# Optimization experiments

Measured on AMD Instinct MI355X. Metric: run time of the kernel, lower is better.

The kernel has to match this reference:

```python
import jax, jax.numpy as jnp
import numpy as np

B, N, C = 4, 2048, 1024
H = 16
D = C // H  # head dim = 64

def setup_inputs() -> dict:
    key = jax.random.key(0)
    k1, k2, k3 = jax.random.split(key, 3)
    x = jax.random.normal(k1, (B, N, C), dtype=jnp.float32)
    w_attn = jax.random.normal(k2, (C, 3 * C), dtype=jnp.float32) * (C ** -0.5)
    w_proj = jax.random.normal(k3, (C, C), dtype=jnp.float32) * (C ** -0.5)
    return {"x": x, "w_attn": w_attn, "w_proj": w_proj}

def reference(x, w_attn, w_proj):
    # fused QKV projection (bias=False)
    qkv = jnp.einsum('bnc,cf->bnf', x, w_attn)            # [B,N,3C]
    q, k, v = jnp.split(qkv, 3, axis=-1)                  # each [B,N,C]
    # [B,H,N,D]
    q = q.reshape(B, N, H, D).transpose(0, 2, 1, 3)
    k = k.reshape(B, N, H, D).transpose(0, 2, 1, 3)
    v = v.reshape(B, N, H, D).transpose(0, 2, 1, 3)
    # scaled dot-product attention, non-causal, no mask, dropout_p=0
    scale = 1.0 / jnp.sqrt(jnp.asarray(D, dtype=q.dtype))
    scores = jnp.einsum('bhqd,bhkd->bhqk', q, k) * scale  # [B,H,N,N]
    attn = jax.nn.softmax(scores, axis=-1)
    y = jnp.einsum('bhqk,bhkd->bhqd', attn, v)            # [B,H,N,D]
    y = y.transpose(0, 2, 1, 3).reshape(B, N, C)
    # output projection (bias=False); resid dropout is identity at p=0
    return jnp.einsum('bnc,co->bno', y, w_proj)
```

## Files before the change

### kernel.cpp

```cpp
#include <hip/hip_runtime.h>
#include <hip/hip_bf16.h>

typedef __hip_bfloat16 bf16;
typedef short short8 __attribute__((ext_vector_type(8)));
typedef float f32x4 __attribute__((ext_vector_type(4)));
typedef float f32x16 __attribute__((ext_vector_type(16)));

#define GLOBAL_AS __attribute__((address_space(1)))
#define LDS_AS __attribute__((address_space(3)))

__device__ inline unsigned short f2bf(float x) {
    union { float f; unsigned u; } v; v.f = x;
    unsigned r = v.u + 0x7fffu + ((v.u >> 16) & 1u);
    return (unsigned short)(r >> 16);
}

__device__ inline unsigned pkbf(float a, float b) {
    float2 f; f.x = a; f.y = b;
    union { __hip_bfloat162 h; unsigned u; } c;
    c.h = __float22bfloat162_rn(f);
    return c.u;
}

__device__ inline float fast_exp2(float x) {
#if __has_builtin(__builtin_amdgcn_exp2f)
    return __builtin_amdgcn_exp2f(x);
#else
    return exp2f(x);
#endif
}

__device__ inline void async16(const void* g, void* l) {
    __builtin_amdgcn_global_load_lds((const GLOBAL_AS void*)g, (LDS_AS void*)l, 16, 0, 0);
}


__global__ __launch_bounds__(256) void cvt_f32_bf16(const float* __restrict__ in,
                                                    unsigned short* __restrict__ out, int n4) {
    int i = blockIdx.x * 256 + threadIdx.x;
    if (i < n4) {
        float4 v = ((const float4*)in)[i];
        ushort4 o;
        o.x = f2bf(v.x); o.y = f2bf(v.y); o.z = f2bf(v.z); o.w = f2bf(v.w);
        ((ushort4*)out)[i] = o;
    }
}

__global__ __launch_bounds__(256) void transpose_bf16(const float* __restrict__ in,
                                                      unsigned short* __restrict__ out,
                                                      int R, int Cc) {
    __shared__ float s[32][33];
    int tx = threadIdx.x & 31, ty = threadIdx.x >> 5;
    int c0 = blockIdx.x * 32, r0 = blockIdx.y * 32;
#pragma unroll
    for (int i = 0; i < 4; i++)
        s[ty + i * 8][tx] = in[(size_t)(r0 + ty + i * 8) * Cc + c0 + tx];
    __syncthreads();
#pragma unroll
    for (int i = 0; i < 4; i++)
        out[(size_t)(c0 + ty + i * 8) * R + r0 + tx] = f2bf(s[tx][ty + i * 8]);
}


template <int MODE>
__global__ __launch_bounds__(256) void gemm_bf16(const bf16* __restrict__ A,
                                                 const bf16* __restrict__ Bt,
                                                 unsigned short* __restrict__ outQ,
                                                 unsigned short* __restrict__ outK,
                                                 unsigned short* __restrict__ outV,
                                                 float* __restrict__ outF, float qscale) {
    const int KD = 1024;
    __shared__ __align__(16) char smem[34816];
    bf16* sA = (bf16*)smem;
    bf16* sB = (bf16*)(smem + 16384);
    const int t = threadIdx.x;
    const int w = t >> 6, lane = t & 63, l15 = lane & 15, qd = lane >> 4;
    const int bn = blockIdx.x, bm = blockIdx.y;
    const int wm = (w >> 1) * 64, wn = (w & 1) * 64;
    const int sw = l15 & 7;

    f32x4 acc[4][4];
#pragma unroll
    for (int i = 0; i < 4; i++)
#pragma unroll
        for (int j = 0; j < 4; j++) acc[i][j] = (f32x4){0.f, 0.f, 0.f, 0.f};

    const int rsub = lane >> 3;
    const int csrc = ((lane & 7) ^ rsub) << 3;
    const bf16* Ab = A + (size_t)(bm * 128 + w * 32 + rsub) * KD + csrc;
    const bf16* Bb = Bt + (size_t)(bn * 128 + w * 32 + rsub) * KD + csrc;
    bf16* sAw = sA + (w * 32) * 64;
    bf16* sBw = sB + (w * 32) * 64;

    for (int kt = 0; kt < 16; ++kt) {
#pragma unroll
        for (int j = 0; j < 4; ++j) {
            async16(Ab + (size_t)(j * 8) * KD + kt * 64, sAw + j * 512);
            async16(Bb + (size_t)(j * 8) * KD + kt * 64, sBw + j * 512);
        }
        __syncthreads();
#pragma unroll
        for (int ks = 0; ks < 2; ++ks) {
            const int cphys = (((ks * 4 + qd) ^ sw) << 3);
            short8 af[4], bfv[4];
#pragma unroll
            for (int mi = 0; mi < 4; mi++)
                af[mi] = *(const short8*)&sA[(wm + mi * 16 + l15) * 64 + cphys];
#pragma unroll
            for (int ni = 0; ni < 4; ni++)
                bfv[ni] = *(const short8*)&sB[(wn + ni * 16 + l15) * 64 + cphys];
#pragma unroll
            for (int mi = 0; mi < 4; mi++)
#pragma unroll
                for (int ni = 0; ni < 4; ni++)
                    acc[mi][ni] = __builtin_amdgcn_mfma_f32_16x16x32_bf16(af[mi], bfv[ni],
                                                                          acc[mi][ni], 0, 0, 0);
        }
        __syncthreads();
    }

    if (MODE == 0) {
        unsigned short* sC = (unsigned short*)smem;
        const int part = bn >> 3;
        const int hb = (bn & 7) * 2;
        if (part < 2) {
            const float sc = (part == 0) ? qscale : 1.0f;
            unsigned short* dst = (part == 0) ? outQ : outK;
#pragma unroll
            for (int mi = 0; mi < 4; mi++)
#pragma unroll
                for (int ni = 0; ni < 4; ni++)
#pragma unroll
                    for (int r = 0; r < 4; r++)
                        sC[(wm + mi * 16 + qd * 4 + r) * 136 + wn + ni * 16 + l15] =
                            f2bf(acc[mi][ni][r] * sc);
            __syncthreads();
#pragma unroll
            for (int i = 0; i < 8; i++) {
                const int j = t + i * 256;
                const int row = j >> 4, c16 = j & 15;
                uint4 v = *(const uint4*)&sC[row * 136 + c16 * 8];
                const int m = bm * 128 + row;
                const int b = m >> 11, ns = m & 2047;
                const int h = hb + (c16 >> 3);
                const int dd = (c16 & 7) * 8;
                *(uint4*)&dst[((size_t)(b * 16 + h) * 2048 + ns) * 64 + dd] = v;
            }
        } else {
#pragma unroll
            for (int ni = 0; ni < 4; ni++)
#pragma unroll
                for (int mi = 0; mi < 4; mi++) {
                    uint2 pk;
                    pk.x = (unsigned)f2bf(acc[mi][ni][0]) | ((unsigned)f2bf(acc[mi][ni][1]) << 16);
                    pk.y = (unsigned)f2bf(acc[mi][ni][2]) | ((unsigned)f2bf(acc[mi][ni][3]) << 16);
                    *(uint2*)&sC[(wn + ni * 16 + l15) * 136 + wm + mi * 16 + qd * 4] = pk;
                }
            __syncthreads();
            const int m0b = bm * 128;
            const int b = m0b >> 11, ns0 = m0b & 2047;
#pragma unroll
            for (int i = 0; i < 8; i++) {
                const int j = t + i * 256;
                const int f = j >> 4, tc = j & 15;
                uint4 v = *(const uint4*)&sC[f * 136 + tc * 8];
                const int h = hb + (f >> 6), dd = f & 63;
                *(uint4*)&outV[((size_t)(b * 16 + h) * 64 + dd) * 2048 + ns0 + tc * 8] = v;
            }
        }
    } else {
        float* sF = (float*)smem;
#pragma unroll
        for (int pass = 0; pass < 2; ++pass) {
            if (pass) __syncthreads();
            if ((wm >> 6) == pass) {
#pragma unroll
                for (int mi = 0; mi < 4; mi++)
#pragma unroll
                    for (int ni = 0; ni < 4; ni++)
#pragma unroll
                        for (int r = 0; r < 4; r++)
                            sF[(mi * 16 + qd * 4 + r) * 132 + wn + ni * 16 + l15] =
                                acc[mi][ni][r];
            }
            __syncthreads();
#pragma unroll
            for (int i = 0; i < 8; i++) {
                const int j = t + i * 256;
                const int row = j >> 5, c4 = j & 31;
                float4 v = *(const float4*)&sF[row * 132 + c4 * 4];
                *(float4*)&outF[(size_t)(bm * 128 + pass * 64 + row) * 1024 + bn * 128 +
                                c4 * 4] = v;
            }
        }
    }
}


__global__ __launch_bounds__(256) void attn_kernel(const bf16* __restrict__ Q,
                                                   const bf16* __restrict__ K,
                                                   const bf16* __restrict__ Vt,
                                                   bf16* __restrict__ Y) {
    const int blk = blockIdx.x;
    const int bh = (blk & 7) * 8 + (blk >> 6);
    const int qt = (blk >> 3) & 7;
    const int b = bh >> 4, h16 = bh & 15;
    const int t = threadIdx.x, w = t >> 6, lane = t & 63;
    const int c = lane & 31, hl = lane >> 5;
    const int sw = c & 7;

    __shared__ __align__(16) char smem[36864];
    bf16* sK0 = (bf16*)smem;
    bf16* sK1 = (bf16*)(smem + 8192);
    bf16* sV0 = (bf16*)(smem + 16384);
    bf16* sV1 = (bf16*)(smem + 24576);
    bf16* sO = (bf16*)smem;

    const size_t bhbase = (size_t)bh * 2048 * 64;

    short8 qfA[4], qfB[4];
#pragma unroll
    for (int kc = 0; kc < 4; kc++) {
        qfA[kc] = *(const short8*)(Q + bhbase + (size_t)(qt * 256 + w * 64 + c) * 64 +
                                   kc * 16 + hl * 8);
        qfB[kc] = *(const short8*)(Q + bhbase + (size_t)(qt * 256 + w * 64 + 32 + c) * 64 +
                                   kc * 16 + hl * 8);
    }

    f32x16 z16;
#pragma unroll
    for (int i = 0; i < 16; i++) z16[i] = 0.f;
    f32x16 ot[4];
#pragma unroll
    for (int j = 0; j < 4; j++)
#pragma unroll
        for (int i = 0; i < 16; i++) ot[j][i] = 0.f;
    float lA = 0.f, lB = 0.f;

    const int rsub = lane >> 3;
    const int cg = ((lane & 7) ^ rsub) << 3;
    const bf16* Kb = K + bhbase + (size_t)(w * 16 + rsub) * 64 + cg;
    const bf16* Vb = Vt + bhbase + (size_t)(w * 16 + rsub) * 2048 + cg;
    const int ldsoff = (w * 16) * 64;

#define STAGE(ktile, sKb, sVb)                                                      \
    {                                                                               \
        _Pragma("unroll") for (int j = 0; j < 2; j++) {                             \
            async16(Kb + (size_t)(ktile) * 4096 + j * 512, (sKb) + ldsoff + j * 512); \
            async16(Vb + (size_t)(ktile) * 64 + (size_t)j * 16384,                  \
                    (sVb) + ldsoff + j * 512);                                      \
        }                                                                           \
    }

    auto compute = [&](const bf16* __restrict__ sKb, const bf16* __restrict__ sVb) {
#pragma unroll
        for (int kt2 = 0; kt2 < 2; ++kt2) {
            short8 kf[4];
#pragma unroll
            for (int kc = 0; kc < 4; kc++)
                kf[kc] =
                    *(const short8*)&sKb[(kt2 * 32 + c) * 64 + (((kc * 2 + hl) ^ sw) << 3)];
            __builtin_amdgcn_s_setprio(1);
            f32x16 accA = __builtin_amdgcn_mfma_f32_32x32x16_bf16(kf[0], qfA[0], z16, 0, 0, 0);
            f32x16 accB = __builtin_amdgcn_mfma_f32_32x32x16_bf16(kf[0], qfB[0], z16, 0, 0, 0);
#pragma unroll
            for (int kc = 1; kc < 4; kc++) {
                accA = __builtin_amdgcn_mfma_f32_32x32x16_bf16(kf[kc], qfA[kc], accA, 0, 0, 0);
                accB = __builtin_amdgcn_mfma_f32_32x32x16_bf16(kf[kc], qfB[kc], accB, 0, 0, 0);
            }
            __builtin_amdgcn_s_setprio(0);
            unsigned uA[8], uB[8];
            float lsA = 0.f, lsB = 0.f;
#pragma unroll
            for (int i = 0; i < 8; i++) {
                float a0 = fast_exp2(accA[2 * i]);
                float a1 = fast_exp2(accA[2 * i + 1]);
                lsA += a0 + a1;
                uA[i] = pkbf(a0, a1);
                float b0 = fast_exp2(accB[2 * i]);
                float b1 = fast_exp2(accB[2 * i + 1]);
                lsB += b0 + b1;
                uB[i] = pkbf(b0, b1);
            }
            lA += lsA;
            lB += lsB;
            union { uint4 u4; short8 s8; } FA[2], FB[2];
            FA[0].u4.x = uA[0]; FA[0].u4.y = uA[1]; FA[0].u4.z = uA[2]; FA[0].u4.w = uA[3];
            FA[1].u4.x = uA[4]; FA[1].u4.y = uA[5]; FA[1].u4.z = uA[6]; FA[1].u4.w = uA[7];
            FB[0].u4.x = uB[0]; FB[0].u4.y = uB[1]; FB[0].u4.z = uB[2]; FB[0].u4.w = uB[3];
            FB[1].u4.x = uB[4]; FB[1].u4.y = uB[5]; FB[1].u4.z = uB[6]; FB[1].u4.w = uB[7];
            __builtin_amdgcn_s_setprio(1);
#pragma unroll
            for (int g = 0; g < 2; ++g) {
#pragma unroll
                for (int mi2 = 0; mi2 < 2; mi2++) {
                    const bf16* vr = &sVb[(mi2 * 32 + c) * 64];
                    uint2 a0 = *(const uint2*)&vr[(((kt2 * 4 + 2 * g) ^ sw) << 3) + hl * 4];
                    uint2 a1 =
                        *(const uint2*)&vr[(((kt2 * 4 + 2 * g + 1) ^ sw) << 3) + hl * 4];
                    union { uint4 u4; short8 s8; } vf;
                    vf.u4.x = a0.x; vf.u4.y = a0.y; vf.u4.z = a1.x; vf.u4.w = a1.y;
                    ot[mi2] =
                        __builtin_amdgcn_mfma_f32_32x32x16_bf16(vf.s8, FA[g].s8, ot[mi2], 0, 0, 0);
                    ot[2 + mi2] = __builtin_amdgcn_mfma_f32_32x32x16_bf16(vf.s8, FB[g].s8,
                                                                          ot[2 + mi2], 0, 0, 0);
                }
            }
            __builtin_amdgcn_s_setprio(0);
        }
    };

    STAGE(0, sK0, sV0);
    for (int kt = 0; kt < 32; kt += 2) {
        __syncthreads();
        STAGE(kt + 1, sK1, sV1);
        compute(sK0, sV0);
        __syncthreads();
        if (kt + 2 < 32) STAGE(kt + 2, sK0, sV0);
        compute(sK1, sV1);
    }
    __syncthreads();

    float lAt = lA + __shfl_xor(lA, 32, 64);
    float lBt = lB + __shfl_xor(lB, 32, 64);
    float rlA = 1.f / lAt;
    float rlB = 1.f / lBt;
#pragma unroll
    for (int mi2 = 0; mi2 < 2; mi2++)
#pragma unroll
        for (int q4 = 0; q4 < 4; q4++) {
            const int d0 = mi2 * 32 + q4 * 8 + hl * 4;
            uint2 pkA;
            pkA.x = pkbf(ot[mi2][q4 * 4 + 0] * rlA, ot[mi2][q4 * 4 + 1] * rlA);
            pkA.y = pkbf(ot[mi2][q4 * 4 + 2] * rlA, ot[mi2][q4 * 4 + 3] * rlA);
            *(uint2*)&sO[(w * 64 + c) * 72 + d0] = pkA;
            uint2 pkB;
            pkB.x = pkbf(ot[2 + mi2][q4 * 4 + 0] * rlB, ot[2 + mi2][q4 * 4 + 1] * rlB);
            pkB.y = pkbf(ot[2 + mi2][q4 * 4 + 2] * rlB, ot[2 + mi2][q4 * 4 + 3] * rlB);
            *(uint2*)&sO[(w * 64 + 32 + c) * 72 + d0] = pkB;
        }
    __syncthreads();
#pragma unroll
    for (int i = 0; i < 8; i++) {
        int row = (t >> 3) + i * 32, doff = (t & 7) * 8;
        uint4 vv = *(const uint4*)&sO[row * 72 + doff];
        *(uint4*)(Y + ((size_t)(b * 2048 + qt * 256 + row)) * 1024 + h16 * 64 + doff) = vv;
    }
#undef STAGE
}


extern "C" void kernel_launch(void* const* d_in, const int* in_sizes, int n_in,
                              void* d_out, int out_size, void* d_ws, size_t ws_size,
                              hipStream_t stream) {
    const float* x = (const float*)d_in[0];
    const float* w_attn = (const float*)d_in[1];
    const float* w_proj = (const float*)d_in[2];
    float* out = (float*)d_out;
    char* ws = (char*)d_ws;

    bf16* xb = (bf16*)(ws);
    bf16* waT = (bf16*)(ws + 16777216);
    bf16* wpT = (bf16*)(ws + 23068672);
    bf16* qb = (bf16*)(ws + 25165824);
    bf16* kb = (bf16*)(ws + 41943040);
    bf16* vtb = (bf16*)(ws + 58720256);

    cvt_f32_bf16<<<8192, 256, 0, stream>>>(x, (unsigned short*)xb, 2097152);
    transpose_bf16<<<dim3(96, 32), 256, 0, stream>>>(w_attn, (unsigned short*)waT, 1024, 3072);
    transpose_bf16<<<dim3(32, 32), 256, 0, stream>>>(w_proj, (unsigned short*)wpT, 1024, 1024);

    const float qscale = 0.125f * 1.44269504088896340736f;
    gemm_bf16<0><<<dim3(24, 64), 256, 0, stream>>>(xb, waT, (unsigned short*)qb,
                                                   (unsigned short*)kb, (unsigned short*)vtb,
                                                   nullptr, qscale);
    attn_kernel<<<dim3(512), 256, 0, stream>>>(qb, kb, vtb, xb );
    gemm_bf16<1><<<dim3(8, 64), 256, 0, stream>>>(xb, wpT, nullptr, nullptr, nullptr, out, 1.0f);
}
```

Measured before the change: 270.0 us.

## Deepen attention K/V staging to a four-buffer ring with vmcnt waits

Replaces the double-buffered K/V LDS staging in the attention kernel with a four-slot ring that keeps three tiles in flight. Plain __syncthreads barriers become partial s_waitcnt vmcnt waits followed by s_barrier, so later loads can stay outstanding while the current tile is consumed. The aim is to hide more global-load latency behind MFMA compute. LDS use grows from 36KB to 64KB per block, which may lower occupancy, and correctness depends on STAGE issuing exactly four vector loads per tile and on those loads being direct-to-LDS.

```diff
diff --git a/kernel.cpp b/kernel.cpp
--- a/kernel.cpp
+++ b/kernel.cpp
@@ -197,6 +197,10 @@
 }
 
 
+#define WAITV8() asm volatile("s_waitcnt vmcnt(8)" ::: "memory")
+#define WAITV4() asm volatile("s_waitcnt vmcnt(4)" ::: "memory")
+#define WAITV0() asm volatile("s_waitcnt vmcnt(0)" ::: "memory")
+
 __global__ __launch_bounds__(256) void attn_kernel(const bf16* __restrict__ Q,
                                                    const bf16* __restrict__ K,
                                                    const bf16* __restrict__ Vt,
@@ -209,11 +213,11 @@
     const int c = lane & 31, hl = lane >> 5;
     const int sw = c & 7;
 
-    __shared__ __align__(16) char smem[36864];
-    bf16* sK0 = (bf16*)smem;
-    bf16* sK1 = (bf16*)(smem + 8192);
-    bf16* sV0 = (bf16*)(smem + 16384);
-    bf16* sV1 = (bf16*)(smem + 24576);
+    __shared__ __align__(16) char smem[65536];
+    bf16* sKr[4] = {(bf16*)smem, (bf16*)(smem + 8192), (bf16*)(smem + 16384),
+                    (bf16*)(smem + 24576)};
+    bf16* sVr[4] = {(bf16*)(smem + 32768), (bf16*)(smem + 40960), (bf16*)(smem + 49152),
+                    (bf16*)(smem + 57344)};
     bf16* sO = (bf16*)smem;
 
     const size_t bhbase = (size_t)bh * 2048 * 64;
@@ -310,15 +314,35 @@
         }
     };
 
-    STAGE(0, sK0, sV0);
-    for (int kt = 0; kt < 32; kt += 2) {
-        __syncthreads();
-        STAGE(kt + 1, sK1, sV1);
-        compute(sK0, sV0);
-        __syncthreads();
-        if (kt + 2 < 32) STAGE(kt + 2, sK0, sV0);
-        compute(sK1, sV1);
-    }
+    STAGE(0, sKr[0], sVr[0]);
+    STAGE(1, sKr[1], sVr[1]);
+    STAGE(2, sKr[2], sVr[2]);
+#pragma unroll 1
+    for (int tq = 0; tq < 7; ++tq) {
+        const int tb = tq * 4;
+        WAITV8(); __builtin_amdgcn_s_barrier();
+        STAGE(tb + 3, sKr[3], sVr[3]);
+        compute(sKr[0], sVr[0]);
+        WAITV8(); __builtin_amdgcn_s_barrier();
+        STAGE(tb + 4, sKr[0], sVr[0]);
+        compute(sKr[1], sVr[1]);
+        WAITV8(); __builtin_amdgcn_s_barrier();
+        STAGE(tb + 5, sKr[1], sVr[1]);
+        compute(sKr[2], sVr[2]);
+        WAITV8(); __builtin_amdgcn_s_barrier();
+        STAGE(tb + 6, sKr[2], sVr[2]);
+        compute(sKr[3], sVr[3]);
+    }
+    WAITV8(); __builtin_amdgcn_s_barrier();
+    STAGE(31, sKr[3], sVr[3]);
+    compute(sKr[0], sVr[0]);
+    WAITV8(); __builtin_amdgcn_s_barrier();
+    compute(sKr[1], sVr[1]);
+    WAITV4(); __builtin_amdgcn_s_barrier();
+    compute(sKr[2], sVr[2]);
+    WAITV0(); __builtin_amdgcn_s_barrier();
+    compute(sKr[3], sVr[3]);
+
     __syncthreads();
 
     float lAt = lA + __shfl_xor(lA, 32, 64);
```

After: 286.9 us. 6.3% more time.

## Double-buffer GEMM shared-memory tiles with K-step of 32

Applied to the files above, without the earlier changes.

The bf16 GEMM main loop now uses two LDS buffers per operand with 32-wide K tiles, issuing async global-to-LDS loads for the next tile while MFMAs run on the current one. Before, each iteration loaded a 64-wide tile, waited, then computed, so load latency was not hidden. The swizzle changes to match the 32-column layout. The cost is twice as many barriers and half the work per stage.

```diff
diff --git a/kernel.cpp b/kernel.cpp
--- a/kernel.cpp
+++ b/kernel.cpp
@@ -71,13 +71,14 @@
                                                  float* __restrict__ outF, float qscale) {
     const int KD = 1024;
     __shared__ __align__(16) char smem[34816];
-    bf16* sA = (bf16*)smem;
-    bf16* sB = (bf16*)(smem + 16384);
+    bf16* sA0 = (bf16*)smem;
+    bf16* sA1 = (bf16*)(smem + 8192);
+    bf16* sB0 = (bf16*)(smem + 16384);
+    bf16* sB1 = (bf16*)(smem + 24576);
     const int t = threadIdx.x;
     const int w = t >> 6, lane = t & 63, l15 = lane & 15, qd = lane >> 4;
     const int bn = blockIdx.x, bm = blockIdx.y;
     const int wm = (w >> 1) * 64, wn = (w & 1) * 64;
-    const int sw = l15 & 7;
 
     f32x4 acc[4][4];
 #pragma unroll
@@ -85,39 +86,47 @@
 #pragma unroll
         for (int j = 0; j < 4; j++) acc[i][j] = (f32x4){0.f, 0.f, 0.f, 0.f};
 
-    const int rsub = lane >> 3;
-    const int csrc = ((lane & 7) ^ rsub) << 3;
-    const bf16* Ab = A + (size_t)(bm * 128 + w * 32 + rsub) * KD + csrc;
-    const bf16* Bb = Bt + (size_t)(bn * 128 + w * 32 + rsub) * KD + csrc;
-    bf16* sAw = sA + (w * 32) * 64;
-    bf16* sBw = sB + (w * 32) * 64;
-
-    for (int kt = 0; kt < 16; ++kt) {
-#pragma unroll
-        for (int j = 0; j < 4; ++j) {
-            async16(Ab + (size_t)(j * 8) * KD + kt * 64, sAw + j * 512);
-            async16(Bb + (size_t)(j * 8) * KD + kt * 64, sBw + j * 512);
-        }
+    const int rsub4 = lane >> 2;
+    const int csrc = (((lane & 3) ^ (rsub4 & 3)) << 3);
+    const bf16* Ab = A + (size_t)(bm * 128 + w * 32 + rsub4) * KD + csrc;
+    const bf16* Bb = Bt + (size_t)(bn * 128 + w * 32 + rsub4) * KD + csrc;
+    const int ldso = w * 1024;
+
+#define STAGEG(kt, sAb, sBb)                                                       \
+    {                                                                              \
+        _Pragma("unroll") for (int j = 0; j < 2; j++) {                            \
+            async16(Ab + (size_t)(j * 16) * KD + (kt) * 32, (sAb) + ldso + j * 512); \
+            async16(Bb + (size_t)(j * 16) * KD + (kt) * 32, (sBb) + ldso + j * 512); \
+        }                                                                          \
+    }
+
+    const int pg = ((qd ^ (l15 & 3)) << 3);
+    auto computeg = [&](const bf16* __restrict__ sAb, const bf16* __restrict__ sBb) {
+        short8 af[4], bfv[4];
+#pragma unroll
+        for (int mi = 0; mi < 4; mi++)
+            af[mi] = *(const short8*)&sAb[(wm + mi * 16 + l15) * 32 + pg];
+#pragma unroll
+        for (int ni = 0; ni < 4; ni++)
+            bfv[ni] = *(const short8*)&sBb[(wn + ni * 16 + l15) * 32 + pg];
+#pragma unroll
+        for (int mi = 0; mi < 4; mi++)
+#pragma unroll
+            for (int ni = 0; ni < 4; ni++)
+                acc[mi][ni] = __builtin_amdgcn_mfma_f32_16x16x32_bf16(af[mi], bfv[ni],
+                                                                      acc[mi][ni], 0, 0, 0);
+    };
+
+    STAGEG(0, sA0, sB0);
+    for (int kt = 0; kt < 32; kt += 2) {
         __syncthreads();
-#pragma unroll
-        for (int ks = 0; ks < 2; ++ks) {
-            const int cphys = (((ks * 4 + qd) ^ sw) << 3);
-            short8 af[4], bfv[4];
-#pragma unroll
-            for (int mi = 0; mi < 4; mi++)
-                af[mi] = *(const short8*)&sA[(wm + mi * 16 + l15) * 64 + cphys];
-#pragma unroll
-            for (int ni = 0; ni < 4; ni++)
-                bfv[ni] = *(const short8*)&sB[(wn + ni * 16 + l15) * 64 + cphys];
-#pragma unroll
-            for (int mi = 0; mi < 4; mi++)
-#pragma unroll
-                for (int ni = 0; ni < 4; ni++)
-                    acc[mi][ni] = __builtin_amdgcn_mfma_f32_16x16x32_bf16(af[mi], bfv[ni],
-                                                                          acc[mi][ni], 0, 0, 0);
-        }
+        STAGEG(kt + 1, sA1, sB1);
+        computeg(sA0, sB0);
         __syncthreads();
-    }
+        if (kt + 2 < 32) STAGEG(kt + 2, sA0, sB0);
+        computeg(sA1, sB1);
+    }
+    __syncthreads();
 
     if (MODE == 0) {
         unsigned short* sC = (unsigned short*)smem;
@@ -194,6 +203,7 @@
             }
         }
     }
+#undef STAGEG
 }
 
 
```

Result: no change. 272.4 us (+0.9%).
